# Optimization experiments

Hardware: AMD Instinct MI355X
Metric: run time of the kernel (lower is better)

## Reference

```python
import jax, jax.numpy as jnp
import numpy as np

D_MODEL = 1024
N_EXPERTS = 8
TOP_K = 2
B, S = 2, 2048


def setup_inputs() -> dict:
    key = jax.random.key(0)
    ks = jax.random.split(key, 12)
    d, e, h = D_MODEL, N_EXPERTS, 4 * D_MODEL
    sd = 1.0 / np.sqrt(d)
    sh = 1.0 / np.sqrt(h)
    return {
        "x": jax.random.normal(ks[0], (B, S, d), dtype=jnp.float32),
        "noise": jax.random.uniform(ks[1], (B, S, e), dtype=jnp.float32),
        # router linear [d, E]
        "Wr": jax.random.uniform(ks[2], (d, e), minval=-sd, maxval=sd),
        "br": jax.random.uniform(ks[3], (e,), minval=-sd, maxval=sd),
        # noise linear [d, E]
        "Wn": jax.random.uniform(ks[4], (d, e), minval=-sd, maxval=sd),
        "bn": jax.random.uniform(ks[5], (e,), minval=-sd, maxval=sd),
        # stacked expert FFN weights
        "W1": jax.random.uniform(ks[6], (e, d, h), minval=-sd, maxval=sd),
        "b1": jax.random.uniform(ks[7], (e, h), minval=-sd, maxval=sd),
        "W2": jax.random.uniform(ks[8], (e, h, d), minval=-sh, maxval=sh),
        "b2": jax.random.uniform(ks[9], (e, d), minval=-sh, maxval=sh),
    }


def _moe_forward(x, noise, Wr, br, Wn, bn, W1, b1, W2, b2):
    e = Wr.shape[-1]
    # noisy top-k router
    logits = x @ Wr + br + jax.nn.softplus(x @ Wn + bn) * noise  # [B,S,E]
    top_v, top_i = jax.lax.top_k(logits, TOP_K)                  # [B,S,K]
    # softmax over sparse top-k (non-topk entries are -inf -> weight 0)
    gates_k = jax.nn.softmax(top_v, axis=-1)                     # [B,S,K]
    gating = jnp.sum(jax.nn.one_hot(top_i, e, dtype=x.dtype) * gates_k[..., None], axis=-2)  # [B,S,E]
    # experts (dropout in eval mode = identity). Non-selected experts have
    # gate 0, so the dense weighted sum equals the masked gather/scatter.
    hdn = jax.nn.relu(jnp.einsum('bsd,edh->bseh', x, W1) + b1)   # [B,S,E,4d]
    y = jnp.einsum('bseh,ehd->bsed', hdn, W2) + b2               # [B,S,E,d]
    return jnp.einsum('bse,bsed->bsd', gating, y)


def reference(x, noise, Wr, br, Wn, bn, W1, b1, W2, b2):
    return _moe_forward(x, noise, Wr, br, Wn, bn, W1, b1, W2, b2)
```

## Files before the change

kernel.cpp:

```cpp
#include <hip/hip_runtime.h>
#include <hip/hip_bf16.h>
#include <cstdint>
#include <cstddef>

#define D_MODEL 1024
#define N_EXP   8
#define HID     4096
#define T_TOK   4096
#define NPAIR   (T_TOK * 2)
#define WSLOTS  72

#define WS_COUNTS   0
#define WS_CURSOR   32
#define WS_OFFSETS  64
#define WS_TOKE     128
#define WS_TOKG     32896
#define WS_LTOK     65664
#define WS_LGATE    98432
#define WS_XB       131328
#define WS_WB       (WS_XB + 8388608)
#define WS_H        (WS_WB + 67108864)

typedef __attribute__((ext_vector_type(8))) short bf16x8;
typedef __attribute__((ext_vector_type(4))) float f32x4;
typedef __attribute__((ext_vector_type(8))) unsigned short u16x8;
typedef unsigned short u16;

__device__ __forceinline__ u16 f2bf(float f) {
    unsigned u = __float_as_uint(f);
    u += 0x7FFFu + ((u >> 16) & 1u);
    return (u16)(u >> 16);
}

__device__ __forceinline__ void glds16(const void* g, void* l) {
    __builtin_amdgcn_global_load_lds(
        (const __attribute__((address_space(1))) void*)g,
        (__attribute__((address_space(3))) void*)l, 16, 0, 0);
}

__device__ __forceinline__ void chunk_map(int c, int& row, int& kc) {
    const int line = c >> 3, c8 = c & 7, u = c8 ^ (line & 7);
    row = line * 2 + (u >> 2);
    kc  = (u & 3) * 8;
}

__device__ __forceinline__ bool work_map(const int* counts, int w,
                                         int& e, int& m_t) {
    int tot = 0; e = -1; m_t = 0;
    #pragma unroll
    for (int i = 0; i < N_EXP; ++i) {
        const int tl = (counts[i] + 127) >> 7;
        if (e < 0 && w < tot + tl) { e = i; m_t = w - tot; }
        tot += tl;
    }
    return e >= 0;
}

__global__ __launch_bounds__(256) void k_router(
    const float* __restrict__ x, const float* __restrict__ noise,
    const float* __restrict__ Wr, const float* __restrict__ br,
    const float* __restrict__ Wn, const float* __restrict__ bn,
    int* __restrict__ counts, int* __restrict__ tok_e, float* __restrict__ tok_g,
    u16* __restrict__ xb)
{
    const int t   = blockIdx.x;
    const int tid = threadIdx.x;
    const int e   = tid & 7;
    const int g   = tid >> 3;
    const float* xr = x + (size_t)t * D_MODEL;

    {
        const float4 v4 = *(const float4*)(xr + tid * 4);
        ushort4 o;
        o.x = f2bf(v4.x); o.y = f2bf(v4.y); o.z = f2bf(v4.z); o.w = f2bf(v4.w);
        *(ushort4*)(xb + (size_t)t * D_MODEL + tid * 4) = o;
    }

    float ar = 0.f, an = 0.f;
    const int ibase = g * 32;
    #pragma unroll 8
    for (int j = 0; j < 32; ++j) {
        const int i = ibase + j;
        const float xv = xr[i];
        ar = fmaf(xv, Wr[i * 8 + e], ar);
        an = fmaf(xv, Wn[i * 8 + e], an);
    }

    __shared__ float sR[256], sN[256];
    sR[tid] = ar; sN[tid] = an;
    __syncthreads();
    for (int off = 128; off >= 8; off >>= 1) {
        if (tid < off) { sR[tid] += sR[tid + off]; sN[tid] += sN[tid + off]; }
        __syncthreads();
    }

    __shared__ float lg[8];
    if (tid < 8) {
        const float z  = sN[tid] + bn[tid];
        const float sp = fmaxf(z, 0.f) + log1pf(expf(-fabsf(z)));
        lg[tid] = sR[tid] + br[tid] + sp * noise[t * 8 + tid];
    }
    __syncthreads();

    if (tid == 0) {
        float v0 = -INFINITY, v1 = -INFINITY;
        int   i0 = 0,         i1 = 0;
        #pragma unroll
        for (int ee = 0; ee < 8; ++ee) {
            const float v = lg[ee];
            if (v > v0)      { v1 = v0; i1 = i0; v0 = v; i0 = ee; }
            else if (v > v1) { v1 = v;  i1 = ee; }
        }
        const float ew  = expf(v1 - v0);
        const float inv = 1.f / (1.f + ew);
        tok_e[t * 2 + 0] = i0;
        tok_e[t * 2 + 1] = i1;
        tok_g[t * 2 + 0] = inv;
        tok_g[t * 2 + 1] = ew * inv;
        atomicAdd(&counts[i0], 1);
        atomicAdd(&counts[i1], 1);
    }
}

__global__ void k_prefix(const int* __restrict__ counts, int* __restrict__ offsets)
{
    if (threadIdx.x == 0 && blockIdx.x == 0) {
        int acc = 0;
        #pragma unroll
        for (int e = 0; e < N_EXP; ++e) { offsets[e] = acc; acc += counts[e]; }
    }
}

__global__ __launch_bounds__(256) void k_scatter(
    const int* __restrict__ tok_e, const float* __restrict__ tok_g,
    const int* __restrict__ offsets, int* __restrict__ cursor,
    int* __restrict__ list_tok, float* __restrict__ list_gate)
{
    const int gid = blockIdx.x * 256 + threadIdx.x;
    if (gid >= NPAIR) return;
    const int e = tok_e[gid];
    const int p = atomicAdd(&cursor[e], 1);
    const int slot = offsets[e] + p;
    list_tok[slot]  = gid >> 1;
    list_gate[slot] = tok_g[gid];
}

__global__ __launch_bounds__(256) void k_cvtT(
    const float* __restrict__ in, u16* __restrict__ outp, int R, int C)
{
    const size_t esz = (size_t)R * C;
    const float* ine = in + (size_t)blockIdx.z * esz;
    u16* oute = outp + (size_t)blockIdx.z * esz;
    const int c0 = blockIdx.x * 32, r0 = blockIdx.y * 64;

    __shared__ u16 s[64 * 33];
    const int tid = threadIdx.x;
    const int lr = tid >> 3, lc = (tid & 7) * 4;
    #pragma unroll
    for (int p = 0; p < 2; ++p) {
        const int row = lr + p * 32;
        const float4 v = *(const float4*)(ine + (size_t)(r0 + row) * C + c0 + lc);
        s[row * 33 + lc + 0] = f2bf(v.x);
        s[row * 33 + lc + 1] = f2bf(v.y);
        s[row * 33 + lc + 2] = f2bf(v.z);
        s[row * 33 + lc + 3] = f2bf(v.w);
    }
    __syncthreads();
    const int oc = tid >> 3, rr = (tid & 7) * 8;
    u16x8 o;
    #pragma unroll
    for (int i = 0; i < 8; ++i) o[i] = s[(rr + i) * 33 + oc];
    *(u16x8*)(oute + (size_t)(c0 + oc) * R + r0 + rr) = o;
}

__global__ __launch_bounds__(256, 4) void k_ffn1(
    const u16* __restrict__ xb,
    const u16* __restrict__ W1t,
    const float* __restrict__ b1,
    const int* __restrict__ counts, const int* __restrict__ offsets,
    const int* __restrict__ list_tok,
    u16* __restrict__ H)
{
    const int bid = blockIdx.x;
    const int n_t = (bid & 7) | (((bid >> 3) & 3) << 3);
    const int wsl = bid >> 5;

    int e, m_t;
    if (!work_map(counts, wsl, e, m_t)) return;
    const int cnt  = counts[e];
    const int base = offsets[e];
    const int m0   = m_t * 128;
    const int n0   = n_t * 128;
    const u16* __restrict__ Be = W1t + (size_t)e * (HID * D_MODEL);

    __shared__ __align__(16) u16 SA[2 * 4096];
    __shared__ __align__(16) u16 SB[2 * 4096];
    __shared__ int stok[128];

    const int tid = threadIdx.x;
    if (tid < 128) stok[tid] = list_tok[base + min(m0 + tid, cnt - 1)];
    __syncthreads();

    int ar0, ak0, ar1, ak1;
    chunk_map(tid, ar0, ak0);
    chunk_map(tid + 256, ar1, ak1);
    const u16* Asrc0 = xb + (size_t)stok[ar0] * D_MODEL + ak0;
    const u16* Asrc1 = xb + (size_t)stok[ar1] * D_MODEL + ak1;
    const u16* Bsrc0 = Be + (size_t)(n0 + ar0) * D_MODEL + ak0;
    const u16* Bsrc1 = Be + (size_t)(n0 + ar1) * D_MODEL + ak1;

    const int lane = tid & 63, lr = lane & 15, hk = lane >> 4;
    const int w = tid >> 6, wm = w >> 1, wn = w & 1;
    const int colb  = ((((lr & 1) << 2) + hk) ^ (lr >> 1)) << 4;
    const int baseA = ((wm * 32 + (lr >> 1)) << 7) + colb;
    const int baseB = ((wn * 32 + (lr >> 1)) << 7) + colb;

    float bias[4];
    #pragma unroll
    for (int j = 0; j < 4; ++j) bias[j] = b1[(size_t)e * HID + n0 + wn * 64 + j * 16 + lr];

    f32x4 acc[4][4] = {};

    auto STAGE = [&](int s, int t) {
        const int kt = t * 32;
        char* Ab = (char*)SA + s * 8192;
        char* Bb = (char*)SB + s * 8192;
        glds16(Asrc0 + kt, Ab + tid * 16);
        glds16(Asrc1 + kt, Ab + (tid + 256) * 16);
        glds16(Bsrc0 + kt, Bb + tid * 16);
        glds16(Bsrc1 + kt, Bb + (tid + 256) * 16);
    };
    auto COMPUTE = [&](int s) {
        const char* Ab = (const char*)SA + s * 8192;
        const char* Bb = (const char*)SB + s * 8192;
        bf16x8 a[4], b[4];
        #pragma unroll
        for (int i = 0; i < 4; ++i) a[i] = *(const bf16x8*)(Ab + baseA + i * 1024);
        #pragma unroll
        for (int j = 0; j < 4; ++j) b[j] = *(const bf16x8*)(Bb + baseB + j * 1024);
        #pragma unroll
        for (int i = 0; i < 4; ++i)
            #pragma unroll
            for (int j = 0; j < 4; ++j)
                acc[i][j] = __builtin_amdgcn_mfma_f32_16x16x32_bf16(a[i], b[j], acc[i][j], 0, 0, 0);
    };

    const int NT = D_MODEL / 32;
    STAGE(0, 0);
    STAGE(1, 1);
    for (int t = 0; t < NT; ++t) {
        if (t < NT - 1) { asm volatile("s_waitcnt vmcnt(4)" ::: "memory"); }
        else            { asm volatile("s_waitcnt vmcnt(0)" ::: "memory"); }
        __builtin_amdgcn_s_barrier();
        __builtin_amdgcn_sched_barrier(0);
        COMPUTE(t & 1);
        __builtin_amdgcn_sched_barrier(0);
        __builtin_amdgcn_s_barrier();
        if (t + 2 < NT) STAGE(t & 1, t + 2);
    }

    #pragma unroll
    for (int i = 0; i < 4; ++i) {
        #pragma unroll
        for (int g = 0; g < 4; ++g) {
            const int m = m0 + wm * 64 + i * 16 + hk * 4 + g;
            if (m < cnt) {
                u16* dst = H + (size_t)(base + m) * HID + n0 + wn * 64 + lr;
                #pragma unroll
                for (int j = 0; j < 4; ++j)
                    dst[j * 16] = f2bf(fmaxf(acc[i][j][g] + bias[j], 0.f));
            }
        }
    }
}

__global__ __launch_bounds__(256, 4) void k_ffn2(
    const u16* __restrict__ Hb,
    const u16* __restrict__ W2t,
    const float* __restrict__ b2,
    const int* __restrict__ counts, const int* __restrict__ offsets,
    const int* __restrict__ list_tok, const float* __restrict__ list_gate,
    float* __restrict__ out)
{
    const int bid = blockIdx.x;
    const int n_t = bid & 7;
    const int kh  = (bid >> 3) & 1;
    const int wsl = bid >> 4;

    int e, m_t;
    if (!work_map(counts, wsl, e, m_t)) return;
    const int cnt  = counts[e];
    const int base = offsets[e];
    const int m0   = m_t * 128;
    const int n0   = n_t * 128;
    const int k0   = kh * (HID / 2);
    const u16* __restrict__ Be = W2t + (size_t)e * (D_MODEL * HID);

    __shared__ __align__(16) u16 SA[2 * 4096];
    __shared__ __align__(16) u16 SB[2 * 4096];
    __shared__ int   s_tok[128];
    __shared__ float s_gate[128];

    const int tid = threadIdx.x;
    if (tid < 128) {
        const int sl = base + min(m0 + tid, cnt - 1);
        s_tok[tid]  = list_tok[sl];
        s_gate[tid] = list_gate[sl];
    }
    __syncthreads();

    int ar0, ak0, ar1, ak1;
    chunk_map(tid, ar0, ak0);
    chunk_map(tid + 256, ar1, ak1);
    const u16* Asrc0 = Hb + (size_t)(base + min(m0 + ar0, cnt - 1)) * HID + k0 + ak0;
    const u16* Asrc1 = Hb + (size_t)(base + min(m0 + ar1, cnt - 1)) * HID + k0 + ak1;
    const u16* Bsrc0 = Be + (size_t)(n0 + ar0) * HID + k0 + ak0;
    const u16* Bsrc1 = Be + (size_t)(n0 + ar1) * HID + k0 + ak1;

    const int lane = tid & 63, lr = lane & 15, hk = lane >> 4;
    const int w = tid >> 6, wm = w >> 1, wn = w & 1;
    const int colb  = ((((lr & 1) << 2) + hk) ^ (lr >> 1)) << 4;
    const int baseA = ((wm * 32 + (lr >> 1)) << 7) + colb;
    const int baseB = ((wn * 32 + (lr >> 1)) << 7) + colb;

    float bias[4];
    #pragma unroll
    for (int j = 0; j < 4; ++j)
        bias[j] = (kh == 0) ? b2[(size_t)e * D_MODEL + n0 + wn * 64 + j * 16 + lr] : 0.f;

    f32x4 acc[4][4] = {};

    auto STAGE = [&](int s, int t) {
        const int kt = t * 32;
        char* Ab = (char*)SA + s * 8192;
        char* Bb = (char*)SB + s * 8192;
        glds16(Asrc0 + kt, Ab + tid * 16);
        glds16(Asrc1 + kt, Ab + (tid + 256) * 16);
        glds16(Bsrc0 + kt, Bb + tid * 16);
        glds16(Bsrc1 + kt, Bb + (tid + 256) * 16);
    };
    auto COMPUTE = [&](int s) {
        const char* Ab = (const char*)SA + s * 8192;
        const char* Bb = (const char*)SB + s * 8192;
        bf16x8 a[4], b[4];
        #pragma unroll
        for (int i = 0; i < 4; ++i) a[i] = *(const bf16x8*)(Ab + baseA + i * 1024);
        #pragma unroll
        for (int j = 0; j < 4; ++j) b[j] = *(const bf16x8*)(Bb + baseB + j * 1024);
        #pragma unroll
        for (int i = 0; i < 4; ++i)
            #pragma unroll
            for (int j = 0; j < 4; ++j)
                acc[i][j] = __builtin_amdgcn_mfma_f32_16x16x32_bf16(a[i], b[j], acc[i][j], 0, 0, 0);
    };

    const int NT = (HID / 2) / 32;
    STAGE(0, 0);
    STAGE(1, 1);
    for (int t = 0; t < NT; ++t) {
        if (t < NT - 1) { asm volatile("s_waitcnt vmcnt(4)" ::: "memory"); }
        else            { asm volatile("s_waitcnt vmcnt(0)" ::: "memory"); }
        __builtin_amdgcn_s_barrier();
        __builtin_amdgcn_sched_barrier(0);
        COMPUTE(t & 1);
        __builtin_amdgcn_sched_barrier(0);
        __builtin_amdgcn_s_barrier();
        if (t + 2 < NT) STAGE(t & 1, t + 2);
    }

    #pragma unroll
    for (int i = 0; i < 4; ++i) {
        #pragma unroll
        for (int g = 0; g < 4; ++g) {
            const int m = m0 + wm * 64 + i * 16 + hk * 4 + g;
            if (m < cnt) {
                const int   mm = m - m0;
                const int   tk = s_tok[mm];
                const float gt = s_gate[mm];
                float* dst = out + (size_t)tk * D_MODEL + n0 + wn * 64 + lr;
                #pragma unroll
                for (int j = 0; j < 4; ++j)
                    unsafeAtomicAdd(dst + j * 16, gt * (acc[i][j][g] + bias[j]));
            }
        }
    }
}

extern "C" void kernel_launch(void* const* d_in, const int* in_sizes, int n_in,
                              void* d_out, int out_size, void* d_ws, size_t ws_size,
                              hipStream_t stream)
{
    const float* x     = (const float*)d_in[0];
    const float* noise = (const float*)d_in[1];
    const float* Wr    = (const float*)d_in[2];
    const float* br    = (const float*)d_in[3];
    const float* Wn    = (const float*)d_in[4];
    const float* bn    = (const float*)d_in[5];
    const float* W1    = (const float*)d_in[6];
    const float* b1    = (const float*)d_in[7];
    const float* W2    = (const float*)d_in[8];
    const float* b2    = (const float*)d_in[9];
    float* out = (float*)d_out;

    char* ws = (char*)d_ws;
    int*   counts    = (int*)(ws + WS_COUNTS);
    int*   cursor    = (int*)(ws + WS_CURSOR);
    int*   offsets   = (int*)(ws + WS_OFFSETS);
    int*   tok_e     = (int*)(ws + WS_TOKE);
    float* tok_g     = (float*)(ws + WS_TOKG);
    int*   list_tok  = (int*)(ws + WS_LTOK);
    float* list_gate = (float*)(ws + WS_LGATE);
    u16*   xb        = (u16*)(ws + WS_XB);
    u16*   Wb        = (u16*)(ws + WS_WB);
    u16*   Hb        = (u16*)(ws + WS_H);

    hipMemsetAsync(ws, 0, 128, stream);
    hipMemsetAsync(d_out, 0, (size_t)out_size * sizeof(float), stream);

    k_cvtT<<<dim3(HID / 32, D_MODEL / 64, N_EXP), 256, 0, stream>>>(W1, Wb, D_MODEL, HID);
    k_router<<<T_TOK, 256, 0, stream>>>(x, noise, Wr, br, Wn, bn, counts, tok_e, tok_g, xb);
    k_prefix<<<1, 64, 0, stream>>>(counts, offsets);
    k_scatter<<<NPAIR / 256, 256, 0, stream>>>(tok_e, tok_g, offsets, cursor,
                                               list_tok, list_gate);

    k_ffn1<<<32 * WSLOTS, 256, 0, stream>>>(xb, Wb, b1, counts, offsets,
                                            list_tok, Hb);

    k_cvtT<<<dim3(D_MODEL / 32, HID / 64, N_EXP), 256, 0, stream>>>(W2, Wb, HID, D_MODEL);
    k_ffn2<<<8 * 2 * WSLOTS, 256, 0, stream>>>(Hb, Wb, b2, counts, offsets,
                                               list_tok, list_gate, out);
}
```

Before: 461.6 us.

## Enlarge expert GEMM tiles to 256 rows with 512-thread blocks and 4-stage LDS ring

Measured after the change: 518.4 us. 1.12x slower.

```diff
diff --git a/kernel.cpp b/kernel.cpp
--- a/kernel.cpp
+++ b/kernel.cpp
@@ -8,7 +8,7 @@
 #define HID     4096
 #define T_TOK   4096
 #define NPAIR   (T_TOK * 2)
-#define WSLOTS  72
+#define WSL256  40
 
 #define WS_COUNTS   0
 #define WS_CURSOR   32
@@ -44,12 +44,12 @@
     kc  = (u & 3) * 8;
 }
 
-__device__ __forceinline__ bool work_map(const int* counts, int w,
-                                         int& e, int& m_t) {
+__device__ __forceinline__ bool work_map256(const int* counts, int w,
+                                            int& e, int& m_t) {
     int tot = 0; e = -1; m_t = 0;
     #pragma unroll
     for (int i = 0; i < N_EXP; ++i) {
-        const int tl = (counts[i] + 127) >> 7;
+        const int tl = (counts[i] + 255) >> 8;
         if (e < 0 && w < tot + tl) { e = i; m_t = w - tot; }
         tot += tl;
     }
@@ -173,7 +173,7 @@
     *(u16x8*)(oute + (size_t)(c0 + oc) * R + r0 + rr) = o;
 }
 
-__global__ __launch_bounds__(256, 4) void k_ffn1(
+__global__ __launch_bounds__(512, 2) void k_ffn1(
     const u16* __restrict__ xb,
     const u16* __restrict__ W1t,
     const float* __restrict__ b1,
@@ -182,67 +182,84 @@
     u16* __restrict__ H)
 {
     const int bid = blockIdx.x;
-    const int n_t = (bid & 7) | (((bid >> 3) & 3) << 3);
-    const int wsl = bid >> 5;
+    const int n_t = (bid & 7) | (((bid >> 3) & 1) << 3);
+    const int wsl = bid >> 4;
 
     int e, m_t;
-    if (!work_map(counts, wsl, e, m_t)) return;
+    if (!work_map256(counts, wsl, e, m_t)) return;
     const int cnt  = counts[e];
     const int base = offsets[e];
-    const int m0   = m_t * 128;
-    const int n0   = n_t * 128;
+    const int m0   = m_t * 256;
+    const int n0   = n_t * 256;
     const u16* __restrict__ Be = W1t + (size_t)e * (HID * D_MODEL);
 
-    __shared__ __align__(16) u16 SA[2 * 4096];
-    __shared__ __align__(16) u16 SB[2 * 4096];
-    __shared__ int stok[128];
+    __shared__ __align__(16) u16 SA[4 * 8192];
+    __shared__ __align__(16) u16 SB[4 * 8192];
+    __shared__ int stok[256];
 
     const int tid = threadIdx.x;
-    if (tid < 128) stok[tid] = list_tok[base + min(m0 + tid, cnt - 1)];
+    if (tid < 256) stok[tid] = list_tok[base + min(m0 + tid, cnt - 1)];
     __syncthreads();
 
     int ar0, ak0, ar1, ak1;
     chunk_map(tid, ar0, ak0);
-    chunk_map(tid + 256, ar1, ak1);
+    chunk_map(tid + 512, ar1, ak1);
     const u16* Asrc0 = xb + (size_t)stok[ar0] * D_MODEL + ak0;
     const u16* Asrc1 = xb + (size_t)stok[ar1] * D_MODEL + ak1;
     const u16* Bsrc0 = Be + (size_t)(n0 + ar0) * D_MODEL + ak0;
     const u16* Bsrc1 = Be + (size_t)(n0 + ar1) * D_MODEL + ak1;
 
     const int lane = tid & 63, lr = lane & 15, hk = lane >> 4;
-    const int w = tid >> 6, wm = w >> 1, wn = w & 1;
+    const int w = tid >> 6, wm = w >> 2, wn = w & 3;
     const int colb  = ((((lr & 1) << 2) + hk) ^ (lr >> 1)) << 4;
-    const int baseA = ((wm * 32 + (lr >> 1)) << 7) + colb;
+    const int baseA = ((wm * 64 + (lr >> 1)) << 7) + colb;
     const int baseB = ((wn * 32 + (lr >> 1)) << 7) + colb;
 
     float bias[4];
     #pragma unroll
     for (int j = 0; j < 4; ++j) bias[j] = b1[(size_t)e * HID + n0 + wn * 64 + j * 16 + lr];
 
-    f32x4 acc[4][4] = {};
+    f32x4 acc[8][4] = {};
 
     auto STAGE = [&](int s, int t) {
         const int kt = t * 32;
-        char* Ab = (char*)SA + s * 8192;
-        char* Bb = (char*)SB + s * 8192;
+        char* Ab = (char*)SA + s * 16384;
+        char* Bb = (char*)SB + s * 16384;
         glds16(Asrc0 + kt, Ab + tid * 16);
-        glds16(Asrc1 + kt, Ab + (tid + 256) * 16);
+        glds16(Asrc1 + kt, Ab + (tid + 512) * 16);
         glds16(Bsrc0 + kt, Bb + tid * 16);
-        glds16(Bsrc1 + kt, Bb + (tid + 256) * 16);
+        glds16(Bsrc1 + kt, Bb + (tid + 512) * 16);
     };
     auto COMPUTE = [&](int s) {
-        const char* Ab = (const char*)SA + s * 8192;
-        const char* Bb = (const char*)SB + s * 8192;
-        bf16x8 a[4], b[4];
-        #pragma unroll
-        for (int i = 0; i < 4; ++i) a[i] = *(const bf16x8*)(Ab + baseA + i * 1024);
+        const char* Ab = (const char*)SA + s * 16384;
+        const char* Bb = (const char*)SB + s * 16384;
+        bf16x8 b[4];
         #pragma unroll
         for (int j = 0; j < 4; ++j) b[j] = *(const bf16x8*)(Bb + baseB + j * 1024);
-        #pragma unroll
-        for (int i = 0; i < 4; ++i)
+        {
+            bf16x8 a[4];
             #pragma unroll
-            for (int j = 0; j < 4; ++j)
-                acc[i][j] = __builtin_amdgcn_mfma_f32_16x16x32_bf16(a[i], b[j], acc[i][j], 0, 0, 0);
+            for (int i = 0; i < 4; ++i) a[i] = *(const bf16x8*)(Ab + baseA + i * 1024);
+            __builtin_amdgcn_s_setprio(1);
+            #pragma unroll
+            for (int i = 0; i < 4; ++i)
+                #pragma unroll
+                for (int j = 0; j < 4; ++j)
+                    acc[i][j] = __builtin_amdgcn_mfma_f32_16x16x32_bf16(a[i], b[j], acc[i][j], 0, 0, 0);
+            __builtin_amdgcn_s_setprio(0);
+        }
+        {
+            bf16x8 a[4];
+            #pragma unroll
+            for (int i = 0; i < 4; ++i) a[i] = *(const bf16x8*)(Ab + baseA + (i + 4) * 1024);
+            __builtin_amdgcn_s_setprio(1);
+            #pragma unroll
+            for (int i = 0; i < 4; ++i)
+                #pragma unroll
+                for (int j = 0; j < 4; ++j)
+                    acc[i + 4][j] = __builtin_amdgcn_mfma_f32_16x16x32_bf16(a[i], b[j], acc[i + 4][j], 0, 0, 0);
+            __builtin_amdgcn_s_setprio(0);
+        }
     };
 
     const int NT = D_MODEL / 32;
@@ -253,17 +270,16 @@
         else            { asm volatile("s_waitcnt vmcnt(0)" ::: "memory"); }
         __builtin_amdgcn_s_barrier();
         __builtin_amdgcn_sched_barrier(0);
-        COMPUTE(t & 1);
+        if (t + 2 < NT) STAGE((t + 2) & 3, t + 2);
         __builtin_amdgcn_sched_barrier(0);
-        __builtin_amdgcn_s_barrier();
-        if (t + 2 < NT) STAGE(t & 1, t + 2);
-    }
-
-    #pragma unroll
-    for (int i = 0; i < 4; ++i) {
+        COMPUTE(t & 3);
+    }
+
+    #pragma unroll
+    for (int i = 0; i < 8; ++i) {
         #pragma unroll
         for (int g = 0; g < 4; ++g) {
-            const int m = m0 + wm * 64 + i * 16 + hk * 4 + g;
+            const int m = m0 + wm * 128 + i * 16 + hk * 4 + g;
             if (m < cnt) {
                 u16* dst = H + (size_t)(base + m) * HID + n0 + wn * 64 + lr;
                 #pragma unroll
@@ -274,7 +290,7 @@
     }
 }
 
-__global__ __launch_bounds__(256, 4) void k_ffn2(
+__global__ __launch_bounds__(512, 2) void k_ffn2(
     const u16* __restrict__ Hb,
     const u16* __restrict__ W2t,
     const float* __restrict__ b2,
@@ -288,21 +304,21 @@
     const int wsl = bid >> 4;
 
     int e, m_t;
-    if (!work_map(counts, wsl, e, m_t)) return;
+    if (!work_map256(counts, wsl, e, m_t)) return;
     const int cnt  = counts[e];
     const int base = offsets[e];
-    const int m0   = m_t * 128;
+    const int m0   = m_t * 256;
     const int n0   = n_t * 128;
     const int k0   = kh * (HID / 2);
     const u16* __restrict__ Be = W2t + (size_t)e * (D_MODEL * HID);
 
-    __shared__ __align__(16) u16 SA[2 * 4096];
-    __shared__ __align__(16) u16 SB[2 * 4096];
-    __shared__ int   s_tok[128];
-    __shared__ float s_gate[128];
+    __shared__ __align__(16) u16 SA[4 * 8192];
+    __shared__ __align__(16) u16 SB[4 * 4096];
+    __shared__ int   s_tok[256];
+    __shared__ float s_gate[256];
 
     const int tid = threadIdx.x;
-    if (tid < 128) {
+    if (tid < 256) {
         const int sl = base + min(m0 + tid, cnt - 1);
         s_tok[tid]  = list_tok[sl];
         s_gate[tid] = list_gate[sl];
@@ -311,11 +327,10 @@
 
     int ar0, ak0, ar1, ak1;
     chunk_map(tid, ar0, ak0);
-    chunk_map(tid + 256, ar1, ak1);
+    chunk_map(tid + 512, ar1, ak1);
     const u16* Asrc0 = Hb + (size_t)(base + min(m0 + ar0, cnt - 1)) * HID + k0 + ak0;
     const u16* Asrc1 = Hb + (size_t)(base + min(m0 + ar1, cnt - 1)) * HID + k0 + ak1;
-    const u16* Bsrc0 = Be + (size_t)(n0 + ar0) * HID + k0 + ak0;
-    const u16* Bsrc1 = Be + (size_t)(n0 + ar1) * HID + k0 + ak1;
+    const u16* Bsrc  = Be + (size_t)(n0 + ar0) * HID + k0 + ak0;
 
     const int lane = tid & 63, lr = lane & 15, hk = lane >> 4;
     const int w = tid >> 6, wm = w >> 1, wn = w & 1;
@@ -332,40 +347,40 @@
 
     auto STAGE = [&](int s, int t) {
         const int kt = t * 32;
-        char* Ab = (char*)SA + s * 8192;
+        char* Ab = (char*)SA + s * 16384;
         char* Bb = (char*)SB + s * 8192;
         glds16(Asrc0 + kt, Ab + tid * 16);
-        glds16(Asrc1 + kt, Ab + (tid + 256) * 16);
-        glds16(Bsrc0 + kt, Bb + tid * 16);
-        glds16(Bsrc1 + kt, Bb + (tid + 256) * 16);
+        glds16(Asrc1 + kt, Ab + (tid + 512) * 16);
+        glds16(Bsrc  + kt, Bb + tid * 16);
     };
     auto COMPUTE = [&](int s) {
-        const char* Ab = (const char*)SA + s * 8192;
+        const char* Ab = (const char*)SA + s * 16384;
         const char* Bb = (const char*)SB + s * 8192;
         bf16x8 a[4], b[4];
         #pragma unroll
         for (int i = 0; i < 4; ++i) a[i] = *(const bf16x8*)(Ab + baseA + i * 1024);
         #pragma unroll
         for (int j = 0; j < 4; ++j) b[j] = *(const bf16x8*)(Bb + baseB + j * 1024);
+        __builtin_amdgcn_s_setprio(1);
         #pragma unroll
         for (int i = 0; i < 4; ++i)
             #pragma unroll
             for (int j = 0; j < 4; ++j)
                 acc[i][j] = __builtin_amdgcn_mfma_f32_16x16x32_bf16(a[i], b[j], acc[i][j], 0, 0, 0);
+        __builtin_amdgcn_s_setprio(0);
     };
 
     const int NT = (HID / 2) / 32;
     STAGE(0, 0);
     STAGE(1, 1);
     for (int t = 0; t < NT; ++t) {
-        if (t < NT - 1) { asm volatile("s_waitcnt vmcnt(4)" ::: "memory"); }
+        if (t < NT - 1) { asm volatile("s_waitcnt vmcnt(3)" ::: "memory"); }
         else            { asm volatile("s_waitcnt vmcnt(0)" ::: "memory"); }
         __builtin_amdgcn_s_barrier();
         __builtin_amdgcn_sched_barrier(0);
-        COMPUTE(t & 1);
+        if (t + 2 < NT) STAGE((t + 2) & 3, t + 2);
         __builtin_amdgcn_sched_barrier(0);
-        __builtin_amdgcn_s_barrier();
-        if (t + 2 < NT) STAGE(t & 1, t + 2);
+        COMPUTE(t & 3);
     }
 
     #pragma unroll
@@ -423,10 +438,10 @@
     k_scatter<<<NPAIR / 256, 256, 0, stream>>>(tok_e, tok_g, offsets, cursor,
                                                list_tok, list_gate);
 
-    k_ffn1<<<32 * WSLOTS, 256, 0, stream>>>(xb, Wb, b1, counts, offsets,
+    k_ffn1<<<16 * WSL256, 512, 0, stream>>>(xb, Wb, b1, counts, offsets,
                                             list_tok, Hb);
 
     k_cvtT<<<dim3(D_MODEL / 32, HID / 64, N_EXP), 256, 0, stream>>>(W2, Wb, HID, D_MODEL);
-    k_ffn2<<<8 * 2 * WSLOTS, 256, 0, stream>>>(Hb, Wb, b2, counts, offsets,
+    k_ffn2<<<8 * 2 * WSL256, 512, 0, stream>>>(Hb, Wb, b2, counts, offsets,
                                                list_tok, list_gate, out);
 }
```
